# Optimization experiments

Hardware: AMD Instinct MI355X
Metric: run time of the kernel (lower is better)

The kernel has to match this reference:

```python
import jax, jax.numpy as jnp
import numpy as np

B, T, OMNI_D, STATIC_D = 128, 1024, 32, 16
H = 64            # hidden // 2 (per-direction GRU size)
HID = 128         # hidden
PHYS_LEN, N_PHYS = 432, 5


def _gelu(x):
    return jax.nn.gelu(x, approximate=False)  # torch GELU default = exact erf


def _ln(x, g, b, eps=1e-5):
    m = jnp.mean(x, -1, keepdims=True)
    v = jnp.var(x, -1, keepdims=True)
    return (x - m) / jnp.sqrt(v + eps) * g + b


def _gru_layer(x, Wih, Whh, bih, bhh, reverse):
    # PyTorch GRU cell math; x: [B,T,D] -> (outputs [B,T,H], h_final [B,H])
    Hh = Whh.shape[1]
    gi = jnp.einsum('btd,gd->btg', x, Wih) + bih  # precompute input projections
    if reverse:
        gi = gi[:, ::-1]
    gi = jnp.swapaxes(gi, 0, 1)  # [T,B,3H]
    h0 = jnp.zeros((x.shape[0], Hh), x.dtype)

    def step(h, g):
        gh = h @ Whh.T + bhh
        r = jax.nn.sigmoid(g[:, :Hh] + gh[:, :Hh])
        z = jax.nn.sigmoid(g[:, Hh:2 * Hh] + gh[:, Hh:2 * Hh])
        n = jnp.tanh(g[:, 2 * Hh:] + r * gh[:, 2 * Hh:])
        hn = (1 - z) * n + z * h
        return hn, hn

    hT, ys = jax.lax.scan(step, h0, gi)
    ys = jnp.swapaxes(ys, 0, 1)
    if reverse:
        ys = ys[:, ::-1]
    return ys, hT


def _conv1d(x, W, b, pad, dil):
    y = jax.lax.conv_general_dilated(x, W, (1,), [(pad, pad)], rhs_dilation=(dil,),
                                     dimension_numbers=('NCH', 'OIH', 'NCH'))
    return y + b[None, :, None]


def setup_inputs():
    key = jax.random.key(0)
    ks = iter(jax.random.split(key, 64))

    def rn(shape, s=0.05):
        return jax.random.normal(next(ks), shape, jnp.float32) * s

    inp = {
        'omni_seq': rn((B, T, OMNI_D), 1.0),
        'static_x': rn((B, STATIC_D), 1.0),
        'phys': rn((B, N_PHYS, PHYS_LEN), 1.0),
    }
    for l, d_in in (('l0', OMNI_D), ('l1', 2 * H)):
        for dr in ('f', 'b'):
            inp[f'gru_Wih_{l}{dr}'] = rn((3 * H, d_in))
            inp[f'gru_Whh_{l}{dr}'] = rn((3 * H, H))
            inp[f'gru_bih_{l}{dr}'] = rn((3 * H,))
            inp[f'gru_bhh_{l}{dr}'] = rn((3 * H,))
    inp['sm_W'] = rn((H, STATIC_D)); inp['sm_b'] = rn((H,))
    inp['sm_ln_g'] = jnp.ones((H,), jnp.float32); inp['sm_ln_b'] = jnp.zeros((H,), jnp.float32)
    inp['gate_W'] = rn((N_PHYS, H)); inp['gate_b'] = rn((N_PHYS,))
    inp['attn_in_W'] = rn((3 * N_PHYS, N_PHYS)); inp['attn_in_b'] = rn((3 * N_PHYS,))
    inp['attn_out_W'] = rn((N_PHYS, N_PHYS)); inp['attn_out_b'] = rn((N_PHYS,))
    for i, ksz in ((1, 3), (2, 5), (3, 9)):
        inp[f'conv{i}_W'] = rn((HID // 4, N_PHYS, ksz)); inp[f'conv{i}_b'] = rn((HID // 4,))
    FUSED = HID + H + 3 * (HID // 4)  # 288
    inp['head_ln_g'] = jnp.ones((FUSED,), jnp.float32); inp['head_ln_b'] = jnp.zeros((FUSED,), jnp.float32)
    inp['head_W1'] = rn((HID, FUSED)); inp['head_b1'] = rn((HID,))
    inp['head_W2'] = rn((PHYS_LEN, HID)); inp['head_b2'] = rn((PHYS_LEN,))
    return inp


def reference(omni_seq, static_x, phys,
              gru_Wih_l0f, gru_Whh_l0f, gru_bih_l0f, gru_bhh_l0f,
              gru_Wih_l0b, gru_Whh_l0b, gru_bih_l0b, gru_bhh_l0b,
              gru_Wih_l1f, gru_Whh_l1f, gru_bih_l1f, gru_bhh_l1f,
              gru_Wih_l1b, gru_Whh_l1b, gru_bih_l1b, gru_bhh_l1b,
              sm_W, sm_b, sm_ln_g, sm_ln_b, gate_W, gate_b,
              attn_in_W, attn_in_b, attn_out_W, attn_out_b,
              conv1_W, conv1_b, conv2_W, conv2_b, conv3_W, conv3_b,
              head_ln_g, head_ln_b, head_W1, head_b1, head_W2, head_b2):
    # --- bidirectional 2-layer GRU (eval mode: dropout off) ---
    y0f, _ = _gru_layer(omni_seq, gru_Wih_l0f, gru_Whh_l0f, gru_bih_l0f, gru_bhh_l0f, False)
    y0b, _ = _gru_layer(omni_seq, gru_Wih_l0b, gru_Whh_l0b, gru_bih_l0b, gru_bhh_l0b, True)
    x1 = jnp.concatenate([y0f, y0b], -1)
    _, hf = _gru_layer(x1, gru_Wih_l1f, gru_Whh_l1f, gru_bih_l1f, gru_bhh_l1f, False)
    _, hb = _gru_layer(x1, gru_Wih_l1b, gru_Whh_l1b, gru_bih_l1b, gru_bhh_l1b, True)
    omni_embed = jnp.concatenate([hf, hb], -1)  # h_omni[-2] ++ h_omni[-1], [B,128]
    # --- static MLP ---
    static_embed = _ln(_gelu(static_x @ sm_W.T + sm_b), sm_ln_g, sm_ln_b)  # [B,64]
    # --- gating on phys channels ---
    gates = jax.nn.sigmoid(static_embed @ gate_W.T + gate_b)[..., None]  # [B,5,1]
    p = phys * gates  # [B,5,432]
    # --- tiny MHA: embed_dim=5, 5 heads, head_dim=1 -> scale = 1/sqrt(1) = 1 ---
    pt = jnp.swapaxes(p, 1, 2)  # [B,432,5]
    qkv = pt @ attn_in_W.T + attn_in_b
    E = N_PHYS
    q, k, v = qkv[..., :E], qkv[..., E:2 * E], qkv[..., 2 * E:]
    scores = jnp.einsum('bih,bjh->bhij', q, k)  # [B,5,432,432]
    attn = jax.nn.softmax(scores, -1)
    ao = jnp.einsum('bhij,bjh->bih', attn, v)
    ao = ao @ attn_out_W.T + attn_out_b  # out_proj
    p = jnp.swapaxes(ao, 1, 2)  # [B,5,432]
    # --- dilated conv branches + GELU + adaptive avg pool (= mean over length) ---
    c1 = _gelu(_conv1d(p, conv1_W, conv1_b, 1, 1)).mean(-1)
    c2 = _gelu(_conv1d(p, conv2_W, conv2_b, 2, 2)).mean(-1)
    c3 = _gelu(_conv1d(p, conv3_W, conv3_b, 4, 4)).mean(-1)
    fused = jnp.concatenate([omni_embed, static_embed, c1, c2, c3], 1)  # [B,288]
    h = _ln(fused, head_ln_g, head_ln_b)
    h = _gelu(h @ head_W1.T + head_b1)  # dropout off in eval
    return h @ head_W2.T + head_b2  # [B,432]
```

## Files before the change

### kernel.cpp

```cpp
#include <hip/hip_runtime.h>
#include <stdint.h>

#define B_ 128
#define T_ 1024
#define BT_ (B_*T_)
#define H_ 64
#define G_ 192
#define PL_ 432
#define NP_ 5
#define FUSED_ 288
#define N_IN 41

typedef unsigned short u16;
typedef __attribute__((ext_vector_type(8))) short bf16x8;
typedef __attribute__((ext_vector_type(4))) float f32x4;
typedef _Float16 h2 __attribute__((ext_vector_type(2)));
typedef _Float16 h8 __attribute__((ext_vector_type(8)));

__device__ inline float bf2f(u16 u){ union{float f; unsigned int i;} c; c.i = ((unsigned int)u)<<16; return c.f; }
__device__ inline u16 f2bf(float f){ unsigned int u = __float_as_uint(f); unsigned int r = (u + 0x7fffu + ((u>>16)&1u))>>16; return (u16)r; }
__device__ inline _Float16 bf2h(u16 u){ return (_Float16)bf2f(u); }
__device__ inline float sigm(float x){ return 1.f/(1.f+__expf(-x)); }
__device__ inline float tanh_(float x){ float t = __expf(fminf(fmaxf(2.f*x,-30.f),30.f)); return (t-1.f)/(t+1.f); }
__device__ inline float gelu_(float x){ return 0.5f*x*(1.f + erff(x*0.70710678118654752f)); }
__device__ inline float wredsum(float v){
  #pragma unroll
  for(int o=32;o>0;o>>=1) v += __shfl_xor(v,o);
  return v;
}

#if __has_builtin(__builtin_amdgcn_fdot2)
__device__ inline float dot2(h2 a, h2 b, float c){ return __builtin_amdgcn_fdot2(a, b, c, false); }
#else
__device__ inline float dot2(h2 a, h2 b, float c){ return c + (float)a.x*(float)b.x + (float)a.y*(float)b.y; }
#endif

struct CvtArgs {
  const void* src[N_IN];
  unsigned dstOff[N_IN];
  unsigned cnt[N_IN];
  unsigned blkStart[N_IN+1];
};

__global__ __launch_bounds__(256) void convert_k(CvtArgs a, u16* __restrict__ dst){
  const bool isbf = (((const u16*)a.src[21])[0] == 0x3F80u);
  int b = blockIdx.x;
  int lo = 0, hi = N_IN;
  while (hi - lo > 1){ int mid = (lo+hi)>>1; if (a.blkStart[mid] <= (unsigned)b) lo = mid; else hi = mid; }
  const int i = lo;
  const unsigned lb = (unsigned)b - a.blkStart[i];
  const unsigned n = a.cnt[i];
  u16* d = dst + a.dstOff[i];
  if (isbf){
    const u16* s = (const u16*)a.src[i];
    #pragma unroll
    for(int e=0;e<8;e++){ unsigned idx = lb*2048u + e*256u + threadIdx.x; if (idx < n) d[idx] = s[idx]; }
  } else {
    const float* s = (const float*)a.src[i];
    #pragma unroll
    for(int e=0;e<8;e++){ unsigned idx = lb*2048u + e*256u + threadIdx.x; if (idx < n) d[idx] = f2bf(s[idx]); }
  }
}

template<int K>
__global__ __launch_bounds__(256) void gi_gemm(const u16* __restrict__ A,
    const u16* __restrict__ Wf, const u16* __restrict__ Wb,
    const u16* __restrict__ biasF, const u16* __restrict__ biasB,
    u16* __restrict__ out)
{
  const int wv = threadIdx.x >> 6, lane = threadIdx.x & 63;
  const int l15 = lane & 15, quad = lane >> 4;
  const size_t mBase = (size_t)blockIdx.x*64 + wv*16;

  bf16x8 afr[K/32];
  #pragma unroll
  for(int kc=0;kc<K/32;kc++)
    afr[kc] = *(const bf16x8*)(A + (mBase + l15)*K + kc*32 + quad*8);

  #pragma unroll
  for(int half=0; half<2; ++half){
    const u16* W    = half ? Wb : Wf;
    const u16* bias = half ? biasB : biasF;
    u16* o = out + (size_t)half * BT_ * G_;
    for(int nt=0; nt<12; ++nt){
      int n = nt*16 + l15;
      f32x4 acc = {0.f,0.f,0.f,0.f};
      #pragma unroll
      for(int kc=0;kc<K/32;kc++){
        bf16x8 bfr = *(const bf16x8*)(W + n*K + kc*32 + quad*8);
        acc = __builtin_amdgcn_mfma_f32_16x16x32_bf16(afr[kc], bfr, acc, 0,0,0);
      }
      float bv = bf2f(bias[n]);
      #pragma unroll
      for(int r=0;r<4;r++){
        size_t row = mBase + quad*4 + r;
        o[row*G_ + n] = f2bf(acc[r] + bv);
      }
    }
  }
}

__global__ __launch_bounds__(64)
__attribute__((amdgpu_waves_per_eu(1,1)))
void recur(const u16* __restrict__ gi,
    const u16* __restrict__ WhF, const u16* __restrict__ WhB,
    const u16* __restrict__ bhF, const u16* __restrict__ bhB,
    u16* __restrict__ y_x1, float* __restrict__ hfin, int layer)
{
  const int chain = blockIdx.x;
  const int dir = chain >> 7;
  const int b = chain & 127;
  const int j = threadIdx.x;
  const u16* Wh = dir ? WhB : WhF;
  const u16* bh = dir ? bhB : bhF;

  h2 wr[32], wz[32], wn[32];
  #pragma unroll
  for(int k8=0;k8<8;k8++){
    uint4 q;
    q = *(const uint4*)(Wh + (size_t)j*64 + k8*8);
    wr[4*k8+0] = (h2){bf2h((u16)(q.x&0xffffu)), bf2h((u16)(q.x>>16))};
    wr[4*k8+1] = (h2){bf2h((u16)(q.y&0xffffu)), bf2h((u16)(q.y>>16))};
    wr[4*k8+2] = (h2){bf2h((u16)(q.z&0xffffu)), bf2h((u16)(q.z>>16))};
    wr[4*k8+3] = (h2){bf2h((u16)(q.w&0xffffu)), bf2h((u16)(q.w>>16))};
    q = *(const uint4*)(Wh + (size_t)(64+j)*64 + k8*8);
    wz[4*k8+0] = (h2){bf2h((u16)(q.x&0xffffu)), bf2h((u16)(q.x>>16))};
    wz[4*k8+1] = (h2){bf2h((u16)(q.y&0xffffu)), bf2h((u16)(q.y>>16))};
    wz[4*k8+2] = (h2){bf2h((u16)(q.z&0xffffu)), bf2h((u16)(q.z>>16))};
    wz[4*k8+3] = (h2){bf2h((u16)(q.w&0xffffu)), bf2h((u16)(q.w>>16))};
    q = *(const uint4*)(Wh + (size_t)(128+j)*64 + k8*8);
    wn[4*k8+0] = (h2){bf2h((u16)(q.x&0xffffu)), bf2h((u16)(q.x>>16))};
    wn[4*k8+1] = (h2){bf2h((u16)(q.y&0xffffu)), bf2h((u16)(q.y>>16))};
    wn[4*k8+2] = (h2){bf2h((u16)(q.z&0xffffu)), bf2h((u16)(q.z>>16))};
    wn[4*k8+3] = (h2){bf2h((u16)(q.w&0xffffu)), bf2h((u16)(q.w>>16))};
  }
  const float bhr = bf2f(bh[j]), bhz = bf2f(bh[64+j]), bhn = bf2f(bh[128+j]);

  __shared__ __align__(16) u16 giLds[2][3072];
  __shared__ _Float16 hSf[64];
  h8* hS8 = (h8*)hSf;
  hSf[j] = (_Float16)0.f;

  const u16* giC = gi + (size_t)chain * T_ * G_;

  auto issue_chunk = [&](int c, int buf){
    int tbase = dir ? (1008 - c*16) : (c*16);
    const u16* src = giC + (size_t)tbase*G_ + j*8;
    u16* dst = &giLds[buf][0];
    #pragma unroll
    for(int i=0;i<6;i++){
      __builtin_amdgcn_global_load_lds(
        (const __attribute__((address_space(1))) void*)(src + i*512),
        (__attribute__((address_space(3))) void*)(dst + i*512), 16, 0, 0);
    }
  };

  issue_chunk(0, 0);

  float h = 0.f;
  for(int c=0; c<64; ++c){
    asm volatile("s_waitcnt vmcnt(0)" ::: "memory");
    if (c < 63) issue_chunk(c+1, (c+1)&1);
    const u16* gbuf = &giLds[c&1][0];
    #pragma unroll 2
    for(int ls=0; ls<16; ++ls){
      int row = dir ? (15-ls) : ls;
      const u16* rowp = gbuf + row*G_;
      float r0=bhr, r1=0.f, z0=bhz, z1=0.f, n0=bhn, n1=0.f;
      #pragma unroll
      for(int k=0;k<8;k++){
        h8 hv = hS8[k];
        h2 p0 = __builtin_shufflevector(hv, hv, 0, 1);
        h2 p1 = __builtin_shufflevector(hv, hv, 2, 3);
        h2 p2 = __builtin_shufflevector(hv, hv, 4, 5);
        h2 p3 = __builtin_shufflevector(hv, hv, 6, 7);
        r0 = dot2(wr[4*k+0], p0, r0); r1 = dot2(wr[4*k+1], p1, r1);
        r0 = dot2(wr[4*k+2], p2, r0); r1 = dot2(wr[4*k+3], p3, r1);
        z0 = dot2(wz[4*k+0], p0, z0); z1 = dot2(wz[4*k+1], p1, z1);
        z0 = dot2(wz[4*k+2], p2, z0); z1 = dot2(wz[4*k+3], p3, z1);
        n0 = dot2(wn[4*k+0], p0, n0); n1 = dot2(wn[4*k+1], p1, n1);
        n0 = dot2(wn[4*k+2], p2, n0); n1 = dot2(wn[4*k+3], p3, n1);
      }
      float gr = bf2f(rowp[j]), gz = bf2f(rowp[64+j]), gn = bf2f(rowp[128+j]);

      float r  = sigm(gr + (r0+r1));
      float z  = sigm(gz + (z0+z1));
      float nn = tanh_(gn + r*(n0+n1));
      h = (1.f - z)*nn + z*h;

      hSf[j] = (_Float16)h;

      if (layer == 0){
        int s = c*16 + ls;
        int t = dir ? (T_-1-s) : s;
        y_x1[((size_t)b*T_ + t)*128 + dir*64 + j] = f2bf(h);
      }
    }
  }
  if (layer == 1) hfin[b*FUSED_ + dir*64 + j] = h;
}

__global__ __launch_bounds__(64) void static_k(const u16* __restrict__ sx,
   const u16* __restrict__ smW, const u16* __restrict__ smb,
   const u16* __restrict__ lng, const u16* __restrict__ lnb,
   const u16* __restrict__ gW, const u16* __restrict__ gb,
   float* __restrict__ fused, float* __restrict__ gates)
{
  int b = blockIdx.x, j = threadIdx.x;
  float xr[16];
  #pragma unroll
  for(int k=0;k<16;k++) xr[k] = bf2f(sx[b*16+k]);
  float acc = bf2f(smb[j]);
  #pragma unroll
  for(int k=0;k<16;k++) acc += xr[k]*bf2f(smW[j*16+k]);
  float xg = gelu_(acc);
  float m = wredsum(xg)*(1.f/64.f);
  float d = xg - m;
  float v = wredsum(d*d)*(1.f/64.f);
  float se = d*rsqrtf(v+1e-5f)*bf2f(lng[j]) + bf2f(lnb[j]);
  fused[b*FUSED_ + 128 + j] = se;
  #pragma unroll
  for(int i=0;i<5;i++){
    float p = se*bf2f(gW[i*64+j]);
    float s = wredsum(p);
    if (j == 0) gates[b*5+i] = sigm(s + bf2f(gb[i]));
  }
}

__global__ __launch_bounds__(448) void qkv_k(const u16* __restrict__ phys,
   const float* __restrict__ gates, const u16* __restrict__ aW,
   const u16* __restrict__ ab, float* __restrict__ qkv)
{
  int b = blockIdx.x, l = threadIdx.x;
  if (l >= PL_) return;
  float pv[5];
  #pragma unroll
  for(int i=0;i<5;i++) pv[i] = bf2f(phys[((size_t)b*5+i)*PL_ + l]) * gates[b*5+i];
  #pragma unroll
  for(int c=0;c<15;c++){
    float a = bf2f(ab[c]);
    #pragma unroll
    for(int i=0;i<5;i++) a += pv[i]*bf2f(aW[c*5+i]);
    qkv[((size_t)b*15+c)*PL_ + l] = a;
  }
}

__global__ __launch_bounds__(256) void attn_k(const float* __restrict__ qkv,
                                              float* __restrict__ ao)
{
  int h = blockIdx.x, b = blockIdx.y;
  int tid = threadIdx.x;
  __shared__ float kS[PL_], vS[PL_];
  __shared__ float red[32];
  const float* qb = qkv + ((size_t)b*15 + h)*PL_;
  const float* kb = qkv + ((size_t)b*15 + 5 + h)*PL_;
  const float* vb = qkv + ((size_t)b*15 + 10 + h)*PL_;
  for(int j=tid;j<PL_;j+=256){ kS[j]=kb[j]; vS[j]=vb[j]; }
  __syncthreads();
  float lmax=-1e30f, lmin=1e30f;
  for(int j=tid;j<PL_;j+=256){ float kv=kS[j]; lmax=fmaxf(lmax,kv); lmin=fminf(lmin,kv); }
  #pragma unroll
  for(int o=32;o>0;o>>=1){ lmax=fmaxf(lmax,__shfl_xor(lmax,o)); lmin=fminf(lmin,__shfl_xor(lmin,o)); }
  int wv = tid>>6;
  if ((tid&63)==0){ red[wv]=lmax; red[8+wv]=lmin; }
  __syncthreads();
  if (tid==0){
    float mx=red[0], mn=red[8];
    for(int i=1;i<4;i++){ mx=fmaxf(mx,red[i]); mn=fminf(mn,red[8+i]); }
    red[16]=mx; red[17]=mn;
  }
  __syncthreads();
  float kmx=red[16], kmn=red[17];
  for(int i=tid;i<PL_;i+=256){
    float s = qb[i];
    float m = fmaxf(s*kmx, s*kmn);
    float den=0.f, num=0.f;
    #pragma unroll 4
    for(int j=0;j<PL_;j++){
      float e = __expf(s*kS[j]-m);
      den += e; num += e*vS[j];
    }
    ao[((size_t)b*PL_+i)*5 + h] = num/den;
  }
}

__global__ __launch_bounds__(448) void proj_k(const float* __restrict__ ao,
   const u16* __restrict__ oW, const u16* __restrict__ ob, float* __restrict__ p2)
{
  int b = blockIdx.x, l = threadIdx.x;
  if (l >= PL_) return;
  float a[5];
  #pragma unroll
  for(int hh=0;hh<5;hh++) a[hh] = ao[((size_t)b*PL_+l)*5 + hh];
  #pragma unroll
  for(int c=0;c<5;c++){
    float s = bf2f(ob[c]);
    #pragma unroll
    for(int hh=0;hh<5;hh++) s += a[hh]*bf2f(oW[c*5+hh]);
    p2[((size_t)b*5+c)*PL_ + l] = s;
  }
}

template<int KS, int DIL, int PAD>
__device__ inline void do_conv(const float* pS, const u16* Wc, const u16* bc,
                               float* fused, int b, int o, int p, int cslot)
{
  const int Lout = PL_ + 2*PAD - DIL*(KS-1);
  float w[5][KS];
  #pragma unroll
  for(int i=0;i<5;i++)
    #pragma unroll
    for(int t=0;t<KS;t++) w[i][t] = bf2f(Wc[(o*5+i)*KS + t]);
  float bias = bf2f(bc[o]);
  float acc = 0.f;
  for(int l=p; l<Lout; l+=8){
    float s = bias;
    #pragma unroll
    for(int t=0;t<KS;t++){
      int idx = l - PAD + t*DIL;
      if (idx >= 0 && idx < PL_){
        #pragma unroll
        for(int i=0;i<5;i++) s += w[i][t]*pS[i*PL_ + idx];
      }
    }
    acc += gelu_(s);
  }
  #pragma unroll
  for(int off=1;off<8;off<<=1) acc += __shfl_xor(acc,off);
  if (p == 0) fused[b*FUSED_ + 192 + cslot*32 + o] = acc/(float)Lout;
}

__global__ __launch_bounds__(256) void conv_k(const float* __restrict__ p2,
  const u16* __restrict__ W1c, const u16* __restrict__ b1c,
  const u16* __restrict__ W2c, const u16* __restrict__ b2c,
  const u16* __restrict__ W3c, const u16* __restrict__ b3c,
  float* __restrict__ fused)
{
  int b = blockIdx.x;
  __shared__ float pS[5*PL_];
  for(int idx=threadIdx.x; idx<5*PL_; idx+=256) pS[idx] = p2[(size_t)b*5*PL_ + idx];
  __syncthreads();
  int o = threadIdx.x >> 3, p = threadIdx.x & 7;
  do_conv<3,1,1>(pS, W1c, b1c, fused, b, o, p, 0);
  do_conv<5,2,2>(pS, W2c, b2c, fused, b, o, p, 1);
  do_conv<9,4,4>(pS, W3c, b3c, fused, b, o, p, 2);
}

__global__ __launch_bounds__(448) void head_k(const float* __restrict__ fused,
   const u16* __restrict__ lng, const u16* __restrict__ lnb,
   const u16* __restrict__ W1, const u16* __restrict__ b1,
   const u16* __restrict__ W2, const u16* __restrict__ b2,
   void* __restrict__ out, const u16* __restrict__ detect)
{
  const bool isbf = (detect[0] == 0x3F80u);
  int b = blockIdx.x, tid = threadIdx.x;
  __shared__ float fS[FUSED_];
  __shared__ float hS[128];
  __shared__ float red[32];
  float v = (tid < FUSED_) ? fused[b*FUSED_ + tid] : 0.f;
  float s1 = wredsum(v);
  float s2 = wredsum(v*v);
  int wv = tid>>6;
  if ((tid&63)==0){ red[wv]=s1; red[8+wv]=s2; }
  __syncthreads();
  if (tid==0){
    float S=0.f, SS=0.f;
    for(int i=0;i<7;i++){ S+=red[i]; SS+=red[8+i]; }
    float m = S/288.f;
    red[16]=m; red[17]=SS/288.f - m*m;
  }
  __syncthreads();
  float m = red[16], var = red[17];
  if (tid < FUSED_) fS[tid] = (v-m)*rsqrtf(var+1e-5f)*bf2f(lng[tid]) + bf2f(lnb[tid]);
  __syncthreads();
  if (tid < 128){
    float a = bf2f(b1[tid]);
    const u16* wr = W1 + (size_t)tid*FUSED_;
    #pragma unroll
    for(int k8=0;k8<36;k8++){
      uint4 q = *(const uint4*)(wr + k8*8);
      a += fS[8*k8+0]*bf2f((u16)(q.x&0xffffu)) + fS[8*k8+1]*bf2f((u16)(q.x>>16))
         + fS[8*k8+2]*bf2f((u16)(q.y&0xffffu)) + fS[8*k8+3]*bf2f((u16)(q.y>>16))
         + fS[8*k8+4]*bf2f((u16)(q.z&0xffffu)) + fS[8*k8+5]*bf2f((u16)(q.z>>16))
         + fS[8*k8+6]*bf2f((u16)(q.w&0xffffu)) + fS[8*k8+7]*bf2f((u16)(q.w>>16));
    }
    hS[tid] = gelu_(a);
  }
  __syncthreads();
  if (tid < PL_){
    float a = bf2f(b2[tid]);
    const u16* wr = W2 + (size_t)tid*128;
    #pragma unroll
    for(int k8=0;k8<16;k8++){
      uint4 q = *(const uint4*)(wr + k8*8);
      a += hS[8*k8+0]*bf2f((u16)(q.x&0xffffu)) + hS[8*k8+1]*bf2f((u16)(q.x>>16))
         + hS[8*k8+2]*bf2f((u16)(q.y&0xffffu)) + hS[8*k8+3]*bf2f((u16)(q.y>>16))
         + hS[8*k8+4]*bf2f((u16)(q.z&0xffffu)) + hS[8*k8+5]*bf2f((u16)(q.z>>16))
         + hS[8*k8+6]*bf2f((u16)(q.w&0xffffu)) + hS[8*k8+7]*bf2f((u16)(q.w>>16));
    }
    size_t oi = (size_t)b*PL_ + tid;
    if (isbf) ((u16*)out)[oi] = f2bf(a);
    else      ((float*)out)[oi] = a;
  }
}

extern "C" void kernel_launch(void* const* d_in, const int* in_sizes, int n_in,
                              void* d_out, int out_size, void* d_ws, size_t ws_size,
                              hipStream_t stream)
{
  static const unsigned cnts[N_IN] = {
    4194304, 2048, 276480,
    6144, 12288, 192, 192,
    6144, 12288, 192, 192,
    24576, 12288, 192, 192,
    24576, 12288, 192, 192,
    1024, 64, 64, 64,
    320, 5,
    75, 15,
    25, 5,
    480, 32, 800, 32, 1440, 32,
    288, 288,
    36864, 128, 55296, 432
  };

  char* ws = (char*)d_ws;
  size_t off = 0;
  auto alloc = [&](size_t bytes){ size_t o = off; off = (off + bytes + 255) & ~(size_t)255; return o; };

  CvtArgs ca;
  const u16* cin[N_IN];
  unsigned totalBlocks = 0;
  for (int i=0;i<N_IN;i++){
    ca.src[i] = d_in[i];
    ca.cnt[i] = cnts[i];
    size_t o = alloc((size_t)cnts[i]*2);
    ca.dstOff[i] = (unsigned)(o/2);
    cin[i] = (const u16*)(ws + o);
    ca.blkStart[i] = totalBlocks;
    totalBlocks += (cnts[i] + 2047u)/2048u;
  }
  ca.blkStart[N_IN] = totalBlocks;
  u16* canon = (u16*)ws;

  u16*   gi    = (u16*)  (ws + alloc((size_t)2*BT_*G_*2));
  u16*   x1    = (u16*)  (ws + alloc((size_t)BT_*128*2));
  float* fused = (float*)(ws + alloc((size_t)B_*FUSED_*4));
  float* gates = (float*)(ws + alloc((size_t)B_*5*4));
  float* qkv   = (float*)(ws + alloc((size_t)B_*15*PL_*4));
  float* ao    = (float*)(ws + alloc((size_t)B_*PL_*5*4));
  float* p2    = (float*)(ws + alloc((size_t)B_*5*PL_*4));
  (void)ws_size; (void)in_sizes; (void)n_in; (void)out_size;

  convert_k<<<totalBlocks, 256, 0, stream>>>(ca, canon);

  gi_gemm<32><<<BT_/64, 256, 0, stream>>>(cin[0], cin[3], cin[7], cin[5], cin[9], gi);
  recur<<<256, 64, 0, stream>>>(gi, cin[4], cin[8], cin[6], cin[10], x1, nullptr, 0);
  gi_gemm<128><<<BT_/64, 256, 0, stream>>>(x1, cin[11], cin[15], cin[13], cin[17], gi);
  recur<<<256, 64, 0, stream>>>(gi, cin[12], cin[16], cin[14], cin[18], nullptr, fused, 1);
  static_k<<<128, 64, 0, stream>>>(cin[1], cin[19], cin[20], cin[21], cin[22], cin[23], cin[24], fused, gates);
  qkv_k<<<128, 448, 0, stream>>>(cin[2], gates, cin[25], cin[26], qkv);
  attn_k<<<dim3(5,128), 256, 0, stream>>>(qkv, ao);
  proj_k<<<128, 448, 0, stream>>>(ao, cin[27], cin[28], p2);
  conv_k<<<128, 256, 0, stream>>>(p2, cin[29], cin[30], cin[31], cin[32], cin[33], cin[34], fused);
  head_k<<<128, 448, 0, stream>>>(fused, cin[35], cin[36], cin[37], cin[38], cin[39], cin[40],
                                  d_out, (const u16*)d_in[21]);
}
```

Baseline: 1.261 ms.

## Process two GRU batch chains per recurrence block to share weights and add ILP

Each recurrence block now advances two independent batch sequences at once, reusing the register-resident recurrent weights for both and interleaving their dot products and activations. This halves the grid from 256 to 128 single-wave blocks, which trades parallelism across CUs for instruction-level parallelism within a wave that hides the dependent latency of each step. The risk is that per-step work doubles on a latency-bound serial chain; if the step was not latency-bound, each block simply takes longer while fewer CUs are used.

```diff
diff --git a/kernel.cpp b/kernel.cpp
--- a/kernel.cpp
+++ b/kernel.cpp
@@ -107,9 +107,9 @@
     const u16* __restrict__ bhF, const u16* __restrict__ bhB,
     u16* __restrict__ y_x1, float* __restrict__ hfin, int layer)
 {
-  const int chain = blockIdx.x;
-  const int dir = chain >> 7;
-  const int b = chain & 127;
+  const int blk = blockIdx.x;
+  const int dir = blk >> 6;
+  const int b0 = (blk & 63) * 2;
   const int j = threadIdx.x;
   const u16* Wh = dir ? WhB : WhF;
   const u16* bh = dir ? bhB : bhF;
@@ -136,68 +136,96 @@
   }
   const float bhr = bf2f(bh[j]), bhz = bf2f(bh[64+j]), bhn = bf2f(bh[128+j]);
 
-  __shared__ __align__(16) u16 giLds[2][3072];
-  __shared__ _Float16 hSf[64];
-  h8* hS8 = (h8*)hSf;
-  hSf[j] = (_Float16)0.f;
-
-  const u16* giC = gi + (size_t)chain * T_ * G_;
+  __shared__ __align__(16) u16 giLds[2][2][3072];
+  __shared__ _Float16 hA[64], hB[64];
+  h8* hA8 = (h8*)hA; h8* hB8 = (h8*)hB;
+  hA[j] = (_Float16)0.f; hB[j] = (_Float16)0.f;
+
+  const u16* giC0 = gi + (size_t)(dir*128 + b0    ) * T_ * G_;
+  const u16* giC1 = gi + (size_t)(dir*128 + b0 + 1) * T_ * G_;
 
   auto issue_chunk = [&](int c, int buf){
     int tbase = dir ? (1008 - c*16) : (c*16);
-    const u16* src = giC + (size_t)tbase*G_ + j*8;
-    u16* dst = &giLds[buf][0];
+    const u16* s0 = giC0 + (size_t)tbase*G_ + j*8;
+    const u16* s1 = giC1 + (size_t)tbase*G_ + j*8;
+    u16* d0 = &giLds[buf][0][0];
+    u16* d1 = &giLds[buf][1][0];
     #pragma unroll
     for(int i=0;i<6;i++){
       __builtin_amdgcn_global_load_lds(
-        (const __attribute__((address_space(1))) void*)(src + i*512),
-        (__attribute__((address_space(3))) void*)(dst + i*512), 16, 0, 0);
+        (const __attribute__((address_space(1))) void*)(s0 + i*512),
+        (__attribute__((address_space(3))) void*)(d0 + i*512), 16, 0, 0);
+      __builtin_amdgcn_global_load_lds(
+        (const __attribute__((address_space(1))) void*)(s1 + i*512),
+        (__attribute__((address_space(3))) void*)(d1 + i*512), 16, 0, 0);
     }
   };
 
   issue_chunk(0, 0);
 
-  float h = 0.f;
+  float ha = 0.f, hb_ = 0.f;
   for(int c=0; c<64; ++c){
     asm volatile("s_waitcnt vmcnt(0)" ::: "memory");
     if (c < 63) issue_chunk(c+1, (c+1)&1);
-    const u16* gbuf = &giLds[c&1][0];
-    #pragma unroll 2
+    const u16* g0 = &giLds[c&1][0][0];
+    const u16* g1 = &giLds[c&1][1][0];
     for(int ls=0; ls<16; ++ls){
       int row = dir ? (15-ls) : ls;
-      const u16* rowp = gbuf + row*G_;
-      float r0=bhr, r1=0.f, z0=bhz, z1=0.f, n0=bhn, n1=0.f;
+      const u16* r0p = g0 + row*G_;
+      const u16* r1p = g1 + row*G_;
+      float ar0=bhr, ar1=0.f, az0=bhz, az1=0.f, an0=bhn, an1=0.f;
+      float br0=bhr, br1=0.f, bz0=bhz, bz1=0.f, bn0=bhn, bn1=0.f;
       #pragma unroll
       for(int k=0;k<8;k++){
-        h8 hv = hS8[k];
-        h2 p0 = __builtin_shufflevector(hv, hv, 0, 1);
-        h2 p1 = __builtin_shufflevector(hv, hv, 2, 3);
-        h2 p2 = __builtin_shufflevector(hv, hv, 4, 5);
-        h2 p3 = __builtin_shufflevector(hv, hv, 6, 7);
-        r0 = dot2(wr[4*k+0], p0, r0); r1 = dot2(wr[4*k+1], p1, r1);
-        r0 = dot2(wr[4*k+2], p2, r0); r1 = dot2(wr[4*k+3], p3, r1);
-        z0 = dot2(wz[4*k+0], p0, z0); z1 = dot2(wz[4*k+1], p1, z1);
-        z0 = dot2(wz[4*k+2], p2, z0); z1 = dot2(wz[4*k+3], p3, z1);
-        n0 = dot2(wn[4*k+0], p0, n0); n1 = dot2(wn[4*k+1], p1, n1);
-        n0 = dot2(wn[4*k+2], p2, n0); n1 = dot2(wn[4*k+3], p3, n1);
+        h8 va = hA8[k], vb = hB8[k];
+        h2 a0 = __builtin_shufflevector(va, va, 0, 1);
+        h2 a1 = __builtin_shufflevector(va, va, 2, 3);
+        h2 a2 = __builtin_shufflevector(va, va, 4, 5);
+        h2 a3 = __builtin_shufflevector(va, va, 6, 7);
+        h2 b0v = __builtin_shufflevector(vb, vb, 0, 1);
+        h2 b1v = __builtin_shufflevector(vb, vb, 2, 3);
+        h2 b2v = __builtin_shufflevector(vb, vb, 4, 5);
+        h2 b3v = __builtin_shufflevector(vb, vb, 6, 7);
+        ar0 = dot2(wr[4*k+0], a0, ar0); br0 = dot2(wr[4*k+0], b0v, br0);
+        ar1 = dot2(wr[4*k+1], a1, ar1); br1 = dot2(wr[4*k+1], b1v, br1);
+        ar0 = dot2(wr[4*k+2], a2, ar0); br0 = dot2(wr[4*k+2], b2v, br0);
+        ar1 = dot2(wr[4*k+3], a3, ar1); br1 = dot2(wr[4*k+3], b3v, br1);
+        az0 = dot2(wz[4*k+0], a0, az0); bz0 = dot2(wz[4*k+0], b0v, bz0);
+        az1 = dot2(wz[4*k+1], a1, az1); bz1 = dot2(wz[4*k+1], b1v, bz1);
+        az0 = dot2(wz[4*k+2], a2, az0); bz0 = dot2(wz[4*k+2], b2v, bz0);
+        az1 = dot2(wz[4*k+3], a3, az1); bz1 = dot2(wz[4*k+3], b3v, bz1);
+        an0 = dot2(wn[4*k+0], a0, an0); bn0 = dot2(wn[4*k+0], b0v, bn0);
+        an1 = dot2(wn[4*k+1], a1, an1); bn1 = dot2(wn[4*k+1], b1v, bn1);
+        an0 = dot2(wn[4*k+2], a2, an0); bn0 = dot2(wn[4*k+2], b2v, bn0);
+        an1 = dot2(wn[4*k+3], a3, an1); bn1 = dot2(wn[4*k+3], b3v, bn1);
       }
-      float gr = bf2f(rowp[j]), gz = bf2f(rowp[64+j]), gn = bf2f(rowp[128+j]);
-
-      float r  = sigm(gr + (r0+r1));
-      float z  = sigm(gz + (z0+z1));
-      float nn = tanh_(gn + r*(n0+n1));
-      h = (1.f - z)*nn + z*h;
-
-      hSf[j] = (_Float16)h;
+      float agr = bf2f(r0p[j]), agz = bf2f(r0p[64+j]), agn = bf2f(r0p[128+j]);
+      float bgr = bf2f(r1p[j]), bgz = bf2f(r1p[64+j]), bgn = bf2f(r1p[128+j]);
+
+      float arr = sigm(agr + (ar0+ar1));
+      float brr = sigm(bgr + (br0+br1));
+      float azz = sigm(agz + (az0+az1));
+      float bzz = sigm(bgz + (bz0+bz1));
+      float ann = tanh_(agn + arr*(an0+an1));
+      float bnn = tanh_(bgn + brr*(bn0+bn1));
+      ha  = (1.f - azz)*ann + azz*ha;
+      hb_ = (1.f - bzz)*bnn + bzz*hb_;
+
+      hA[j] = (_Float16)ha;
+      hB[j] = (_Float16)hb_;
 
       if (layer == 0){
         int s = c*16 + ls;
         int t = dir ? (T_-1-s) : s;
-        y_x1[((size_t)b*T_ + t)*128 + dir*64 + j] = f2bf(h);
+        y_x1[((size_t)b0*T_ + t)*128 + dir*64 + j] = f2bf(ha);
+        y_x1[((size_t)(b0+1)*T_ + t)*128 + dir*64 + j] = f2bf(hb_);
       }
     }
   }
-  if (layer == 1) hfin[b*FUSED_ + dir*64 + j] = h;
+  if (layer == 1){
+    hfin[b0*FUSED_ + dir*64 + j] = ha;
+    hfin[(b0+1)*FUSED_ + dir*64 + j] = hb_;
+  }
 }
 
 __global__ __launch_bounds__(64) void static_k(const u16* __restrict__ sx,
@@ -454,9 +482,9 @@
   convert_k<<<totalBlocks, 256, 0, stream>>>(ca, canon);
 
   gi_gemm<32><<<BT_/64, 256, 0, stream>>>(cin[0], cin[3], cin[7], cin[5], cin[9], gi);
-  recur<<<256, 64, 0, stream>>>(gi, cin[4], cin[8], cin[6], cin[10], x1, nullptr, 0);
+  recur<<<128, 64, 0, stream>>>(gi, cin[4], cin[8], cin[6], cin[10], x1, nullptr, 0);
   gi_gemm<128><<<BT_/64, 256, 0, stream>>>(x1, cin[11], cin[15], cin[13], cin[17], gi);
-  recur<<<256, 64, 0, stream>>>(gi, cin[12], cin[16], cin[14], cin[18], nullptr, fused, 1);
+  recur<<<128, 64, 0, stream>>>(gi, cin[12], cin[16], cin[14], cin[18], nullptr, fused, 1);
   static_k<<<128, 64, 0, stream>>>(cin[1], cin[19], cin[20], cin[21], cin[22], cin[23], cin[24], fused, gates);
   qkv_k<<<128, 448, 0, stream>>>(cin[2], gates, cin[25], cin[26], qkv);
   attn_k<<<dim3(5,128), 256, 0, stream>>>(qkv, ao);
```

Result: slower. 1.995 ms (+58.2%).

## Compute GRU hidden-state matvec with bf16 MFMA instead of fp16 dot2

Applied to the files above, without the earlier changes.

Each recurrent step of the GRU kernel now computes the hidden-to-hidden projection with 24 `mfma_f32_16x16x32_bf16` instructions instead of 96 scalar `fdot2` calls per lane. The weights are held as bf16 MFMA B-fragments in registers, and the bias is folded in as the accumulator's initial value. The hidden state is broadcast as the A operand, so all 16 rows compute the same result. Each lane then picks its gate values from the tile that matches its quad. The aim is to cut VALU work on the serial critical path. In exchange it adds MFMA dependency latency, does redundant row work, and stores h in shared memory as bf16 instead of fp16, which lowers its precision.

```diff
diff --git a/kernel.cpp b/kernel.cpp
--- a/kernel.cpp
+++ b/kernel.cpp
@@ -14,12 +14,9 @@
 typedef unsigned short u16;
 typedef __attribute__((ext_vector_type(8))) short bf16x8;
 typedef __attribute__((ext_vector_type(4))) float f32x4;
-typedef _Float16 h2 __attribute__((ext_vector_type(2)));
-typedef _Float16 h8 __attribute__((ext_vector_type(8)));
 
 __device__ inline float bf2f(u16 u){ union{float f; unsigned int i;} c; c.i = ((unsigned int)u)<<16; return c.f; }
 __device__ inline u16 f2bf(float f){ unsigned int u = __float_as_uint(f); unsigned int r = (u + 0x7fffu + ((u>>16)&1u))>>16; return (u16)r; }
-__device__ inline _Float16 bf2h(u16 u){ return (_Float16)bf2f(u); }
 __device__ inline float sigm(float x){ return 1.f/(1.f+__expf(-x)); }
 __device__ inline float tanh_(float x){ float t = __expf(fminf(fmaxf(2.f*x,-30.f),30.f)); return (t-1.f)/(t+1.f); }
 __device__ inline float gelu_(float x){ return 0.5f*x*(1.f + erff(x*0.70710678118654752f)); }
@@ -28,12 +25,6 @@
   for(int o=32;o>0;o>>=1) v += __shfl_xor(v,o);
   return v;
 }
-
-#if __has_builtin(__builtin_amdgcn_fdot2)
-__device__ inline float dot2(h2 a, h2 b, float c){ return __builtin_amdgcn_fdot2(a, b, c, false); }
-#else
-__device__ inline float dot2(h2 a, h2 b, float c){ return c + (float)a.x*(float)b.x + (float)a.y*(float)b.y; }
-#endif
 
 struct CvtArgs {
   const void* src[N_IN];
@@ -111,42 +102,34 @@
   const int dir = chain >> 7;
   const int b = chain & 127;
   const int j = threadIdx.x;
+  const int l15 = j & 15, quad = j >> 4;
   const u16* Wh = dir ? WhB : WhF;
   const u16* bh = dir ? bhB : bhF;
 
-  h2 wr[32], wz[32], wn[32];
-  #pragma unroll
-  for(int k8=0;k8<8;k8++){
-    uint4 q;
-    q = *(const uint4*)(Wh + (size_t)j*64 + k8*8);
-    wr[4*k8+0] = (h2){bf2h((u16)(q.x&0xffffu)), bf2h((u16)(q.x>>16))};
-    wr[4*k8+1] = (h2){bf2h((u16)(q.y&0xffffu)), bf2h((u16)(q.y>>16))};
-    wr[4*k8+2] = (h2){bf2h((u16)(q.z&0xffffu)), bf2h((u16)(q.z>>16))};
-    wr[4*k8+3] = (h2){bf2h((u16)(q.w&0xffffu)), bf2h((u16)(q.w>>16))};
-    q = *(const uint4*)(Wh + (size_t)(64+j)*64 + k8*8);
-    wz[4*k8+0] = (h2){bf2h((u16)(q.x&0xffffu)), bf2h((u16)(q.x>>16))};
-    wz[4*k8+1] = (h2){bf2h((u16)(q.y&0xffffu)), bf2h((u16)(q.y>>16))};
-    wz[4*k8+2] = (h2){bf2h((u16)(q.z&0xffffu)), bf2h((u16)(q.z>>16))};
-    wz[4*k8+3] = (h2){bf2h((u16)(q.w&0xffffu)), bf2h((u16)(q.w>>16))};
-    q = *(const uint4*)(Wh + (size_t)(128+j)*64 + k8*8);
-    wn[4*k8+0] = (h2){bf2h((u16)(q.x&0xffffu)), bf2h((u16)(q.x>>16))};
-    wn[4*k8+1] = (h2){bf2h((u16)(q.y&0xffffu)), bf2h((u16)(q.y>>16))};
-    wn[4*k8+2] = (h2){bf2h((u16)(q.z&0xffffu)), bf2h((u16)(q.z>>16))};
-    wn[4*k8+3] = (h2){bf2h((u16)(q.w&0xffffu)), bf2h((u16)(q.w>>16))};
-  }
-  const float bhr = bf2f(bh[j]), bhz = bf2f(bh[64+j]), bhn = bf2f(bh[128+j]);
-
-  __shared__ __align__(16) u16 giLds[2][3072];
-  __shared__ _Float16 hSf[64];
-  h8* hS8 = (h8*)hSf;
-  hSf[j] = (_Float16)0.f;
+  bf16x8 wf[12][2];
+  #pragma unroll
+  for(int t=0;t<12;t++){
+    #pragma unroll
+    for(int c=0;c<2;c++)
+      wf[t][c] = *(const bf16x8*)(Wh + (size_t)(t*16 + l15)*64 + c*32 + quad*8);
+  }
+  f32x4 bfr[12];
+  #pragma unroll
+  for(int t=0;t<12;t++){
+    float bv = bf2f(bh[t*16 + l15]);
+    bfr[t] = (f32x4){bv, bv, bv, bv};
+  }
+
+  __shared__ __align__(16) u16 giL[2][16*G_];
+  __shared__ __align__(16) u16 hB[64];
+  hB[j] = 0;
 
   const u16* giC = gi + (size_t)chain * T_ * G_;
 
   auto issue_chunk = [&](int c, int buf){
     int tbase = dir ? (1008 - c*16) : (c*16);
     const u16* src = giC + (size_t)tbase*G_ + j*8;
-    u16* dst = &giLds[buf][0];
+    u16* dst = &giL[buf][0];
     #pragma unroll
     for(int i=0;i<6;i++){
       __builtin_amdgcn_global_load_lds(
@@ -161,34 +144,34 @@
   for(int c=0; c<64; ++c){
     asm volatile("s_waitcnt vmcnt(0)" ::: "memory");
     if (c < 63) issue_chunk(c+1, (c+1)&1);
-    const u16* gbuf = &giLds[c&1][0];
+    const u16* gbuf = &giL[c&1][0];
     #pragma unroll 2
     for(int ls=0; ls<16; ++ls){
       int row = dir ? (15-ls) : ls;
       const u16* rowp = gbuf + row*G_;
-      float r0=bhr, r1=0.f, z0=bhz, z1=0.f, n0=bhn, n1=0.f;
+
+      bf16x8 af0 = *(const bf16x8*)(hB + quad*8);
+      bf16x8 af1 = *(const bf16x8*)(hB + 32 + quad*8);
+
+      f32x4 acc[12];
       #pragma unroll
-      for(int k=0;k<8;k++){
-        h8 hv = hS8[k];
-        h2 p0 = __builtin_shufflevector(hv, hv, 0, 1);
-        h2 p1 = __builtin_shufflevector(hv, hv, 2, 3);
-        h2 p2 = __builtin_shufflevector(hv, hv, 4, 5);
-        h2 p3 = __builtin_shufflevector(hv, hv, 6, 7);
-        r0 = dot2(wr[4*k+0], p0, r0); r1 = dot2(wr[4*k+1], p1, r1);
-        r0 = dot2(wr[4*k+2], p2, r0); r1 = dot2(wr[4*k+3], p3, r1);
-        z0 = dot2(wz[4*k+0], p0, z0); z1 = dot2(wz[4*k+1], p1, z1);
-        z0 = dot2(wz[4*k+2], p2, z0); z1 = dot2(wz[4*k+3], p3, z1);
-        n0 = dot2(wn[4*k+0], p0, n0); n1 = dot2(wn[4*k+1], p1, n1);
-        n0 = dot2(wn[4*k+2], p2, n0); n1 = dot2(wn[4*k+3], p3, n1);
+      for(int t=0;t<12;t++){
+        acc[t] = __builtin_amdgcn_mfma_f32_16x16x32_bf16(af0, wf[t][0], bfr[t], 0,0,0);
+        acc[t] = __builtin_amdgcn_mfma_f32_16x16x32_bf16(af1, wf[t][1], acc[t], 0,0,0);
       }
+
+      float pr = (quad==0) ? acc[0][0] : (quad==1) ? acc[1][0] : (quad==2) ? acc[2][0] : acc[3][0];
+      float pz = (quad==0) ? acc[4][0] : (quad==1) ? acc[5][0] : (quad==2) ? acc[6][0] : acc[7][0];
+      float pn = (quad==0) ? acc[8][0] : (quad==1) ? acc[9][0] : (quad==2) ? acc[10][0] : acc[11][0];
+
       float gr = bf2f(rowp[j]), gz = bf2f(rowp[64+j]), gn = bf2f(rowp[128+j]);
 
-      float r  = sigm(gr + (r0+r1));
-      float z  = sigm(gz + (z0+z1));
-      float nn = tanh_(gn + r*(n0+n1));
+      float r  = sigm(gr + pr);
+      float z  = sigm(gz + pz);
+      float nn = tanh_(gn + r*pn);
       h = (1.f - z)*nn + z*h;
 
-      hSf[j] = (_Float16)h;
+      hB[j] = f2bf(h);
 
       if (layer == 0){
         int s = c*16 + ls;
```

Result: slower. 1.446 ms (+14.6%).
